# Optimization experiments

Hardware: AMD Instinct MI355X
Metric: run time of the kernel (lower is better)

## Reference

```python
import jax, jax.numpy as jnp
import numpy as np
from jax import lax

S_INIT = 0.025
ALPHA = 0.98
DELTA = 2.0
R = 0.5
EPS = 1e-6


def setup_inputs() -> dict:
    key = jax.random.key(0)
    k1, _ = jax.random.split(key)
    B, F, T = 32, 128, 8000
    x = jax.random.uniform(k1, (B, F, T), dtype=jnp.float32)  # nonneg mel energies
    log_s = jnp.full((F,), np.log(S_INIT), dtype=jnp.float32)
    return {"x": x, "log_s": log_s}


def _pcen(x, log_s):
    # x: (B, F, T) or (B, C, F, T)
    squeeze = False
    if x.ndim == 3:
        x = x[:, None]  # (B, 1, F, T)
        squeeze = True
    s = jnp.exp(log_s)[None, None, :]  # (1, 1, F), broadcasts over (B, C, F)
    xt = jnp.moveaxis(x, -1, 0)  # (T, B, C, F)
    m0 = xt[0]

    def step(m_prev, x_i):
        m = (1.0 - s) * m_prev + s * x_i
        return m, m

    _, ms = lax.scan(step, m0, xt[1:])  # (T-1, B, C, F)
    M = jnp.concatenate([m0[None], ms], axis=0)  # (T, B, C, F)
    M = jnp.moveaxis(M, 0, -1)  # (B, C, F, T)
    out = (x / (EPS + M) ** ALPHA + DELTA) ** R - DELTA ** R
    return out[:, 0] if squeeze else out.squeeze(1)


def reference(x, log_s):
    return _pcen(x, log_s)
```

## Files before the change

### kernel.cpp

```cpp
#include <hip/hip_runtime.h>


#define T_LEN 8000
#define F_DIM 128
#define NSEQ  4096
#define CHUNK 2048
#define HALO_ITERS 3

typedef __attribute__((ext_vector_type(4))) float vfloat4;

__device__ __forceinline__ float hw_log2(float v) { return __builtin_amdgcn_logf(v); }
__device__ __forceinline__ float hw_exp2(float v) { return __builtin_amdgcn_exp2f(v); }

__device__ __forceinline__ float pcen_out(float xi, float m) {
    float p = hw_exp2(-0.98f * hw_log2(1e-6f + m));
    return __builtin_amdgcn_sqrtf(fmaf(xi, p, 2.0f)) - 1.4142135623730951f;
}

template<int CTRL, int RMASK>
__device__ __forceinline__ float dpp0(float v) {
    return __int_as_float(__builtin_amdgcn_update_dpp(
        0, __float_as_int(v), CTRL, RMASK, 0xF, true));
}

__device__ __forceinline__ float wscan64(float P, float dk1, float dk2, float dk4,
                                         float dk8, float w15, float w31) {
    P = fmaf(dk1, dpp0<0x111, 0xF>(P), P);
    P = fmaf(dk2, dpp0<0x112, 0xF>(P), P);
    P = fmaf(dk4, dpp0<0x114, 0xF>(P), P);
    P = fmaf(dk8, dpp0<0x118, 0xF>(P), P);
    P = fmaf(w15, dpp0<0x142, 0xA>(P), P);
    P = fmaf(w31, dpp0<0x143, 0xC>(P), P);
    return P;
}

__global__ __launch_bounds__(256) void pcen_kernel(const float* __restrict__ x,
                                                   const float* __restrict__ log_s,
                                                   float* __restrict__ out) {
    const int lane  = threadIdx.x & 63;
    const int wid   = blockIdx.x * 4 + (threadIdx.x >> 6);
    const int seq   = wid >> 2;
    const int chunk = wid & 3;
    const int f     = seq & (F_DIM - 1);

    const float* xp = x   + (size_t)seq * T_LEN;
    float*       op = out + (size_t)seq * T_LEN;

    const float s   = hw_exp2(log_s[f] * 1.4426950408889634f);
    const float a   = 1.0f - s;
    const float l2a = hw_log2(a);

    const float a2 = a * a;
    const float a3 = a2 * a;
    const float a4 = a2 * a2;
    const float c0 = a4;
    const float c1 = c0 * c0;
    const float c2 = c1 * c1;
    const float c3 = c2 * c2;
    const float c4 = c3 * c3;
    const float c5 = c4 * c4;
    const float a256 = c5 * c5;
    const float a4l = hw_exp2((float)(4 * lane) * l2a);
    const float al1 = hw_exp2((float)(lane + 1) * l2a);
    const float inv_a4 = 1.0f / a4;
    const float w15 = hw_exp2((float)(4 * ((lane & 15) + 1)) * l2a);
    const float w31 = hw_exp2((float)(4 * ((lane & 31) + 1)) * l2a);

    const int S     = chunk * CHUNK;
    const int halo  = (chunk == 0) ? 0 : HALO_ITERS;
    const int mains = (chunk < 3) ? (CHUNK / 256) : 7;
    const int total = halo + mains;
    const int base  = S - halo * 256;

    float carry = (chunk == 0) ? xp[0] : 0.0f;

    const float4* xv4 = (const float4*)(xp + base);
    vfloat4*      ov4 = (vfloat4*)(op + base);

    float4 p0 = xv4[0 * 64 + lane];
    float4 p1 = xv4[1 * 64 + lane];
    float4 p2 = xv4[2 * 64 + lane];

    #pragma unroll 1
    for (int it = 0; it < total; ++it) {
        float4 xv = p0;
        p0 = p1; p1 = p2;
        if (it + 3 < total) p2 = xv4[(it + 3) * 64 + lane];

        float B0 = s * xv.x;
        float B1 = fmaf(a, B0, s * xv.y);
        float B2 = fmaf(a, B1, s * xv.z);
        float B3 = fmaf(a, B2, s * xv.w);

        float P = wscan64(B3, c0, c1, c2, c3, w15, w31);

        float E = (P - B3) * inv_a4;
        float C = fmaf(a4l, carry, E);

        float P63 = __int_as_float(__builtin_amdgcn_readlane(__float_as_int(P), 63));
        float newcarry = fmaf(a256, carry, P63);

        if (it >= halo) {
            float m0 = fmaf(a,  C, B0);
            float m1 = fmaf(a2, C, B1);
            float m2 = fmaf(a3, C, B2);
            float m3 = fmaf(a4, C, B3);
            vfloat4 o;
            o.x = pcen_out(xv.x, m0);
            o.y = pcen_out(xv.y, m1);
            o.z = pcen_out(xv.z, m2);
            o.w = pcen_out(xv.w, m3);
            __builtin_nontemporal_store(o, &ov4[it * 64 + lane]);
        }
        carry = newcarry;
    }

    if (chunk == 3) {
        const float w15t = hw_exp2((float)((lane & 15) + 1) * l2a);
        const float w31t = hw_exp2((float)((lane & 31) + 1) * l2a);
        float xt = xp[7936 + lane];
        float P = wscan64(s * xt, a, a2, a4, c1, w15t, w31t);
        float m = fmaf(al1, carry, P);
        op[7936 + lane] = pcen_out(xt, m);
    }
}

extern "C" void kernel_launch(void* const* d_in, const int* in_sizes, int n_in,
                              void* d_out, int out_size, void* d_ws, size_t ws_size,
                              hipStream_t stream) {
    const float* x     = (const float*)d_in[0];
    const float* log_s = (const float*)d_in[1];
    float*       out   = (float*)d_out;
    pcen_kernel<<<dim3(NSEQ), dim3(256), 0, stream>>>(x, log_s, out);
}
```

Baseline: 237.5 us.

## Process each sequence with one wave instead of four halo-overlapped chunks

Replaces the four-wave-per-sequence chunked scan, which recomputed halo iterations, with one wave handling a whole 8000-sample sequence serially over 31 iterations plus a tail. It launches 1024 blocks with a swizzled block-to-sequence mapping, deepens the prefetch to four float4 loads, and issues the tail load early. Nontemporal stores become ordinary stores. This removes the redundant halo loads and compute but cuts the wave count fourfold and lengthens each wave's serial dependency chain, which may reduce latency hiding.

```diff
diff --git a/kernel.cpp b/kernel.cpp
--- a/kernel.cpp
+++ b/kernel.cpp
@@ -4,8 +4,7 @@
 #define T_LEN 8000
 #define F_DIM 128
 #define NSEQ  4096
-#define CHUNK 2048
-#define HALO_ITERS 3
+#define MAIN_IT 31
 
 typedef __attribute__((ext_vector_type(4))) float vfloat4;
 
@@ -34,19 +33,31 @@
     return P;
 }
 
-__global__ __launch_bounds__(256) void pcen_kernel(const float* __restrict__ x,
-                                                   const float* __restrict__ log_s,
-                                                   float* __restrict__ out) {
-    const int lane  = threadIdx.x & 63;
-    const int wid   = blockIdx.x * 4 + (threadIdx.x >> 6);
-    const int seq   = wid >> 2;
-    const int chunk = wid & 3;
-    const int f     = seq & (F_DIM - 1);
+__global__ __launch_bounds__(256, 4) void pcen_kernel(const float* __restrict__ x,
+                                                      const float* __restrict__ log_s,
+                                                      float* __restrict__ out) {
+    const int lane = threadIdx.x & 63;
+    const int widx = threadIdx.x >> 6;
+    const int bid  = blockIdx.x;
+    const int swz  = (bid & 7) * 128 + (bid >> 3);
+    const int seq  = swz * 4 + widx;
+    const int f    = seq & (F_DIM - 1);
 
     const float* xp = x   + (size_t)seq * T_LEN;
     float*       op = out + (size_t)seq * T_LEN;
 
-    const float s   = hw_exp2(log_s[f] * 1.4426950408889634f);
+    const float ls = log_s[f];
+
+    const float4* xv4 = (const float4*)xp;
+    vfloat4*      ov4 = (vfloat4*)op;
+
+    float4 p0 = xv4[0 * 64 + lane];
+    float4 p1 = xv4[1 * 64 + lane];
+    float4 p2 = xv4[2 * 64 + lane];
+    float4 p3 = xv4[3 * 64 + lane];
+    float  xt = xp[7936 + lane];
+
+    const float s   = hw_exp2(ls * 1.4426950408889634f);
     const float a   = 1.0f - s;
     const float l2a = hw_log2(a);
 
@@ -61,31 +72,17 @@
     const float c5 = c4 * c4;
     const float a256 = c5 * c5;
     const float a4l = hw_exp2((float)(4 * lane) * l2a);
-    const float al1 = hw_exp2((float)(lane + 1) * l2a);
     const float inv_a4 = 1.0f / a4;
     const float w15 = hw_exp2((float)(4 * ((lane & 15) + 1)) * l2a);
     const float w31 = hw_exp2((float)(4 * ((lane & 31) + 1)) * l2a);
 
-    const int S     = chunk * CHUNK;
-    const int halo  = (chunk == 0) ? 0 : HALO_ITERS;
-    const int mains = (chunk < 3) ? (CHUNK / 256) : 7;
-    const int total = halo + mains;
-    const int base  = S - halo * 256;
-
-    float carry = (chunk == 0) ? xp[0] : 0.0f;
-
-    const float4* xv4 = (const float4*)(xp + base);
-    vfloat4*      ov4 = (vfloat4*)(op + base);
-
-    float4 p0 = xv4[0 * 64 + lane];
-    float4 p1 = xv4[1 * 64 + lane];
-    float4 p2 = xv4[2 * 64 + lane];
+    float carry = __int_as_float(__builtin_amdgcn_readlane(__float_as_int(p0.x), 0));
 
     #pragma unroll 1
-    for (int it = 0; it < total; ++it) {
+    for (int it = 0; it < MAIN_IT; ++it) {
         float4 xv = p0;
-        p0 = p1; p1 = p2;
-        if (it + 3 < total) p2 = xv4[(it + 3) * 64 + lane];
+        p0 = p1; p1 = p2; p2 = p3;
+        if (it + 4 < MAIN_IT) p3 = xv4[(it + 4) * 64 + lane];
 
         float B0 = s * xv.x;
         float B1 = fmaf(a, B0, s * xv.y);
@@ -98,27 +95,24 @@
         float C = fmaf(a4l, carry, E);
 
         float P63 = __int_as_float(__builtin_amdgcn_readlane(__float_as_int(P), 63));
-        float newcarry = fmaf(a256, carry, P63);
+        carry = fmaf(a256, carry, P63);
 
-        if (it >= halo) {
-            float m0 = fmaf(a,  C, B0);
-            float m1 = fmaf(a2, C, B1);
-            float m2 = fmaf(a3, C, B2);
-            float m3 = fmaf(a4, C, B3);
-            vfloat4 o;
-            o.x = pcen_out(xv.x, m0);
-            o.y = pcen_out(xv.y, m1);
-            o.z = pcen_out(xv.z, m2);
-            o.w = pcen_out(xv.w, m3);
-            __builtin_nontemporal_store(o, &ov4[it * 64 + lane]);
-        }
-        carry = newcarry;
+        float m0 = fmaf(a,  C, B0);
+        float m1 = fmaf(a2, C, B1);
+        float m2 = fmaf(a3, C, B2);
+        float m3 = fmaf(a4, C, B3);
+        vfloat4 o;
+        o.x = pcen_out(xv.x, m0);
+        o.y = pcen_out(xv.y, m1);
+        o.z = pcen_out(xv.z, m2);
+        o.w = pcen_out(xv.w, m3);
+        ov4[it * 64 + lane] = o;
     }
 
-    if (chunk == 3) {
+    {
+        const float al1  = hw_exp2((float)(lane + 1) * l2a);
         const float w15t = hw_exp2((float)((lane & 15) + 1) * l2a);
         const float w31t = hw_exp2((float)((lane & 31) + 1) * l2a);
-        float xt = xp[7936 + lane];
         float P = wscan64(s * xt, a, a2, a4, c1, w15t, w31t);
         float m = fmaf(al1, carry, P);
         op[7936 + lane] = pcen_out(xt, m);
@@ -131,5 +125,5 @@
     const float* x     = (const float*)d_in[0];
     const float* log_s = (const float*)d_in[1];
     float*       out   = (float*)d_out;
-    pcen_kernel<<<dim3(NSEQ), dim3(256), 0, stream>>>(x, log_s, out);
+    pcen_kernel<<<dim3(1024), dim3(256), 0, stream>>>(x, log_s, out);
 }
```

Result: no change. 238.0 us (+0.2%).
